# Kernel optimization log

Measured on AMD Instinct MI355X. Metric: run time of the kernel, lower is better.

## Reference

```python
import jax, jax.numpy as jnp
import numpy as np

EPS = 1.1920929e-7  # torch.finfo(float32).eps, default for F.rms_norm
ATTN_SCALE = 0.1
ROPE_BASE = 10000.0


def _rms_norm(x):
    # F.rms_norm over last dim, no learned weight
    return x * jax.lax.rsqrt(jnp.mean(x * x, axis=-1, keepdims=True) + EPS)


def _rotary(x):
    # x: [B, T, H, D]; rotates halves as in the Rotary module
    T, D = x.shape[1], x.shape[3]
    half = D // 2
    inv_freq = 1.0 / (ROPE_BASE ** (jnp.arange(0, D, 2, dtype=jnp.float32) / D))  # [half]
    freqs = jnp.arange(T, dtype=jnp.float32)[:, None] * inv_freq[None, :]          # [T, half]
    cos = jnp.cos(freqs)[None, :, None, :]
    sin = jnp.sin(freqs)[None, :, None, :]
    x1, x2 = x[..., :half], x[..., half:]
    return jnp.concatenate([x1 * cos + x2 * sin, -x1 * sin + x2 * cos], axis=-1)


def setup_inputs() -> dict:
    key = jax.random.key(0)
    ks = jax.random.split(key, 8)
    B, T, dim, H, hd = 2, 2048, 1024, 16, 64
    gate_in = 12
    s = 1.0 / np.sqrt(dim)
    return {
        "x": jax.random.normal(ks[0], (B, T, dim), dtype=jnp.float32),
        "v1": jax.random.normal(ks[1], (B, T, H, hd), dtype=jnp.float32),
        "Wq": jax.random.uniform(ks[2], (dim, dim), jnp.float32, -s, s),
        "Wk": jax.random.uniform(ks[3], (dim, dim), jnp.float32, -s, s),
        "Wv": jax.random.uniform(ks[4], (dim, dim), jnp.float32, -s, s),
        "Wproj": jax.random.uniform(ks[5], (dim, dim), jnp.float32, -s, s),
        "Wg": jax.random.uniform(ks[6], (H, gate_in), jnp.float32,
                                  -1.0 / np.sqrt(gate_in), 1.0 / np.sqrt(gate_in)),
        "lamb": jnp.float32(0.5),
    }


def reference(x, v1, Wq, Wk, Wv, Wproj, Wg, lamb):
    B, T, dim = x.shape
    H, hd = v1.shape[2], v1.shape[3]
    q = (x @ Wq.T).reshape(B, T, H, hd)
    k = (x @ Wk.T).reshape(B, T, H, hd)
    v = (x @ Wv.T).reshape(B, T, H, hd)
    # value-residual mixing
    v = (1.0 - lamb) * v + lamb * v1
    # QK RMSNorm + RoPE
    q = _rotary(_rms_norm(q))
    k = _rotary(_rms_norm(k))
    # causal SDPA with fixed scale
    scores = jnp.einsum('bqhd,bkhd->bhqk', q, k) * ATTN_SCALE
    causal = jnp.tril(jnp.ones((T, T), dtype=bool))
    scores = jnp.where(causal[None, None], scores, jnp.float32(-jnp.inf))
    probs = jax.nn.softmax(scores, axis=-1)
    y = jnp.einsum('bhqk,bkhd->bqhd', probs, v)  # [B, T, H, hd]
    # sigmoid gate from first 12 channels of x
    gate = jax.nn.sigmoid(x[..., :Wg.shape[1]] @ Wg.T)  # [B, T, H]
    y = y * gate[..., None]
    y = y.reshape(B, T, H * hd) @ Wproj.T
    return y
```

## Files before the change

kernel.cpp:

```cpp
#include <hip/hip_runtime.h>
#include <math.h>


#define B_    2
#define T_    2048
#define DIM_  1024
#define H_    16
#define HD_   64
#define NROW  (B_ * T_)
#define EPS_  1.1920929e-07f
#define SCALE_ 0.1f
#define LOG2_10K 13.287712379549449f
#define INV2PI 0.15915494309189535f

typedef unsigned short u16;
typedef unsigned int   u32;
typedef __bf16 bf16x8 __attribute__((ext_vector_type(8)));
typedef __bf16 bf16x2 __attribute__((ext_vector_type(2)));
typedef float  f32x4  __attribute__((ext_vector_type(4)));

__device__ __forceinline__ u16 f2b(float f) {
  u32 u = __float_as_uint(f);
  u += 0x7fffu + ((u >> 16) & 1u);
  return (u16)(u >> 16);
}
__device__ __forceinline__ u32 pk2(float a, float b) {
#if __has_builtin(__builtin_amdgcn_cvt_pk_bf16_f32)
  bf16x2 r = __builtin_amdgcn_cvt_pk_bf16_f32(a, b);
  return __builtin_bit_cast(u32, r);
#else
  return (u32)f2b(a) | ((u32)f2b(b) << 16);
#endif
}
__device__ __forceinline__ void fast_sincos_rev(float rev, float* s, float* c) {
  const float r = rev - floorf(rev);
#if __has_builtin(__builtin_amdgcn_sinf) && __has_builtin(__builtin_amdgcn_cosf)
  *s = __builtin_amdgcn_sinf(r);
  *c = __builtin_amdgcn_cosf(r);
#else
  *s = __sinf(r * 6.283185307179586f);
  *c = __cosf(r * 6.283185307179586f);
#endif
}
#define MFMA16(a,b,c) __builtin_amdgcn_mfma_f32_16x16x32_bf16((a),(b),(c),0,0,0)

typedef const __attribute__((address_space(1))) unsigned char gbuf_t;
typedef __attribute__((address_space(3))) unsigned char lbuf_t;
__device__ __forceinline__ void gload_lds16(const u16* g, unsigned char* l) {
  __builtin_amdgcn_global_load_lds((gbuf_t*)g, (lbuf_t*)l, 16, 0, 0);
}

__global__ __launch_bounds__(256) void convert_all(
    const float* __restrict__ x, const float* __restrict__ Wq,
    const float* __restrict__ Wk, const float* __restrict__ Wv,
    const float* __restrict__ Wp,
    u16* __restrict__ xb, u16* __restrict__ wb ) {
  const int i = blockIdx.x * 256 + threadIdx.x;
  const float* src;
  u16* dst;
  int off;
  if (i < 1048576)       { src = x;  dst = xb;            off = i; }
  else if (i < 1310720)  { src = Wq; dst = wb;            off = i - 1048576; }
  else if (i < 1572864)  { src = Wk; dst = wb + 1048576;  off = i - 1310720; }
  else if (i < 1835008)  { src = Wv; dst = wb + 2097152;  off = i - 1572864; }
  else                   { src = Wp; dst = wb + 3145728;  off = i - 1835008; }
  const float4 f = ((const float4*)src)[off];
  uint2 o;
  o.x = pk2(f.x, f.y);
  o.y = pk2(f.z, f.w);
  ((uint2*)dst)[off] = o;
}

template <bool IS_PROJ>
__global__ __launch_bounds__(256) void gemm_rp(
    const u16* __restrict__ Ab, const u16* __restrict__ Wb,
    u16* __restrict__ qo, u16* __restrict__ ko, u16* __restrict__ vto,
    float* __restrict__ fo, const float* __restrict__ v1,
    const float* __restrict__ lambp) {
  __shared__ __attribute__((aligned(16))) unsigned char sm[49152];
  const int tid  = threadIdx.x;
  const int w    = tid >> 6;
  const int lane = tid & 63;
  const int lo = lane & 15, hi = lane >> 4;
  const int raw = blockIdx.x;
  const int xcd = raw & 7;
  const int jj  = raw >> 3;
  const int m0 = (xcd * 4 + (jj & 3)) << 7;
  const int by = jj >> 2;
  const int mode = IS_PROJ ? 3 : (by >> 3);
  const int n0 = IS_PROJ ? (by << 7) : ((by & 7) << 7);
  const u16* W = IS_PROJ ? Wb : (Wb + (size_t)mode * (DIM_ * DIM_));

  const int wm = w & 1, wn = w >> 1;

  const u16* agA0 = Ab + (size_t)(m0 + (2 * w + 0) * 16 + lo) * DIM_ + (hi << 3);
  const u16* agA1 = Ab + (size_t)(m0 + (2 * w + 1) * 16 + lo) * DIM_ + (hi << 3);
  const u16* agB0 = W  + (size_t)(n0 + (2 * w + 0) * 16 + lo) * DIM_ + (hi << 3);
  const u16* agB1 = W  + (size_t)(n0 + (2 * w + 1) * 16 + lo) * DIM_ + (hi << 3);

  f32x4 acc[4][4];
#pragma unroll
  for (int i = 0; i < 4; ++i)
#pragma unroll
    for (int j = 0; j < 4; ++j) acc[i][j] = (f32x4){0.f, 0.f, 0.f, 0.f};

  {
    unsigned char* ad0 = sm + (2 * w) * 1024;
    gload_lds16(agA0, ad0);
    gload_lds16(agA1, ad0 + 1024);
    gload_lds16(agB0, ad0 + 8192);
    gload_lds16(agB1, ad0 + 9216);
    agA0 += 32; agA1 += 32; agB0 += 32; agB1 += 32;
    unsigned char* ad1 = sm + 16384 + (2 * w) * 1024;
    gload_lds16(agA0, ad1);
    gload_lds16(agA1, ad1 + 1024);
    gload_lds16(agB0, ad1 + 8192);
    gload_lds16(agB1, ad1 + 9216);
    agA0 += 32; agA1 += 32; agB0 += 32; agB1 += 32;
  }

  int cr = 0;
  int cw = 2;
  for (int kc = 0; kc < DIM_; kc += 32) {
    __builtin_amdgcn_sched_barrier(0);
    if (kc + 32 < DIM_) {
      asm volatile("s_waitcnt vmcnt(4)" ::: "memory");
    } else {
      asm volatile("s_waitcnt vmcnt(0)" ::: "memory");
    }
    __builtin_amdgcn_s_barrier();
    __builtin_amdgcn_sched_barrier(0);
    if (kc + 64 < DIM_) {
      unsigned char* ad = sm + cw * 16384 + (2 * w) * 1024;
      gload_lds16(agA0, ad);
      gload_lds16(agA1, ad + 1024);
      gload_lds16(agB0, ad + 8192);
      gload_lds16(agB1, ad + 9216);
      agA0 += 32; agA1 += 32; agB0 += 32; agB1 += 32;
    }
    const unsigned char* Acur = sm + cr * 16384;
    const unsigned char* Bcur = Acur + 8192;
    bf16x8 bfr[4];
#pragma unroll
    for (int nt = 0; nt < 4; ++nt)
      bfr[nt] = *(const bf16x8*)(Bcur + (((wn * 4 + nt) * 64 + lane) << 4));
#pragma unroll
    for (int mt = 0; mt < 4; ++mt) {
      const bf16x8 af = *(const bf16x8*)(Acur + (((wm * 4 + mt) * 64 + lane) << 4));
#pragma unroll
      for (int nt = 0; nt < 4; ++nt)
        acc[mt][nt] = MFMA16(af, bfr[nt], acc[mt][nt]);
    }
    cr = (cr == 2) ? 0 : cr + 1;
    cw = (cw == 2) ? 0 : cw + 1;
  }

  const int head = (n0 >> 6) + wn;
  if (mode <= 1) {
    u16* C = (mode == 0) ? qo : ko;
    const float if0 = exp2f(-(float)lo * (LOG2_10K / 32.f)) * INV2PI;
    const float if1 = exp2f(-(float)(lo + 16) * (LOG2_10K / 32.f)) * INV2PI;
#pragma unroll
    for (int mt = 0; mt < 4; ++mt)
#pragma unroll
      for (int r = 0; r < 4; ++r) {
        float ss = 0.f;
#pragma unroll
        for (int nt = 0; nt < 4; ++nt) { const float v = acc[mt][nt][r]; ss += v * v; }
        ss += __shfl_xor(ss, 1, 64); ss += __shfl_xor(ss, 2, 64);
        ss += __shfl_xor(ss, 4, 64); ss += __shfl_xor(ss, 8, 64);
        const float scl = rsqrtf(ss * (1.f / 64.f) + EPS_);
        const int row_g = m0 + wm * 64 + mt * 16 + hi * 4 + r;
        const float tpos = (float)(row_g & (T_ - 1));
        float sn0, cs0, sn1, cs1;
        fast_sincos_rev(tpos * if0, &sn0, &cs0);
        fast_sincos_rev(tpos * if1, &sn1, &cs1);
        u16* crow = C + (size_t)row_g * DIM_ + head * HD_;
        const float x10 = acc[mt][0][r] * scl, x11 = acc[mt][1][r] * scl;
        const float x20 = acc[mt][2][r] * scl, x21 = acc[mt][3][r] * scl;
        crow[lo]      = f2b(x10 * cs0 + x20 * sn0);
        crow[16 + lo] = f2b(x11 * cs1 + x21 * sn1);
        crow[32 + lo] = f2b(x20 * cs0 - x10 * sn0);
        crow[48 + lo] = f2b(x21 * cs1 - x11 * sn1);
      }
  } else if (mode == 2) {
    const float lam = lambp[0];
#pragma unroll
    for (int mt = 0; mt < 4; ++mt)
#pragma unroll
      for (int r = 0; r < 4; ++r) {
        const int row_g = m0 + wm * 64 + mt * 16 + hi * 4 + r;
        const int bb = row_g >> 11, tt = row_g & (T_ - 1);
        const int bh = bb * H_ + head;
        const float* v1r = v1 + (size_t)row_g * DIM_ + head * HD_;
#pragma unroll
        for (int nt = 0; nt < 4; ++nt) {
          const int d = nt * 16 + lo;
          const float ov = (1.f - lam) * acc[mt][nt][r] + lam * v1r[d];
          vto[((size_t)(bh * HD_ + d)) * T_ + tt] = f2b(ov);
        }
      }
  } else {
#pragma unroll
    for (int mt = 0; mt < 4; ++mt)
#pragma unroll
      for (int r = 0; r < 4; ++r) {
        const int row_g = m0 + wm * 64 + mt * 16 + hi * 4 + r;
        float* orow = fo + (size_t)row_g * DIM_ + n0 + wn * 64;
#pragma unroll
        for (int nt = 0; nt < 4; ++nt) orow[nt * 16 + lo] = acc[mt][nt][r];
      }
  }
}

__global__ __launch_bounds__(256) void gate_kernel(
    const float* __restrict__ x, const float* __restrict__ Wg,
    float* __restrict__ gate) {
  const int id = blockIdx.x * 256 + threadIdx.x;
  const int n = id >> 4, h = id & 15;
  const float* xr = x + (size_t)n * DIM_;
  const float* wr = Wg + h * 12;
  float s = 0.f;
#pragma unroll
  for (int j = 0; j < 12; ++j) s += xr[j] * wr[j];
  gate[id] = 1.f / (1.f + __expf(-s));
}

__global__ __launch_bounds__(256) void attn3(
    const u16* __restrict__ q, const u16* __restrict__ k, const u16* __restrict__ vt,
    const float* __restrict__ gate, u16* __restrict__ y) {
  __shared__ __attribute__((aligned(16))) unsigned char smem[49152];
  const int tid = threadIdx.x;
  const int wv = tid >> 6, lane = tid & 63, lo = lane & 15, hi = lane >> 4;
  const int raw = blockIdx.x;
  const int xcd = raw & 7;
  const int jj  = raw >> 3;
  const int qt = 31 - (jj >> 2);
  const int bh = xcd * 4 + (jj & 3);
  const int b = bh >> 4, h = bh & 15;
  const int qb = qt << 6;

  const int qrow = b * T_ + qb + wv * 16 + lo;
  const u16* qp = q + (size_t)qrow * DIM_ + h * HD_;
  const bf16x8 qf0 = *(const bf16x8*)(qp + hi * 8);
  const bf16x8 qf1 = *(const bf16x8*)(qp + 32 + hi * 8);

  f32x4 o[4];
#pragma unroll
  for (int i = 0; i < 4; ++i) o[i] = (f32x4){0.f, 0.f, 0.f, 0.f};
  float lrun = 0.f;

  const int sl = tid & 63, skh = (tid >> 6) & 1, st0 = tid >> 7;
  const int srow = sl & 15, skk = skh * 32 + ((sl >> 4) << 3);
  const u16* kg0 = k + ((size_t)(b * T_ + st0 * 16 + srow)) * DIM_ + h * HD_ + skk;
  const u16* kg1 = kg0 + (size_t)32 * DIM_;
  const u16* vg0 = vt + ((size_t)(bh * HD_ + st0 * 16 + srow)) * T_ + skk;
  const u16* vg1 = vg0 + (size_t)32 * T_;
  const int wub = (tid >> 6) << 10;

  {
    gload_lds16(kg0, smem + wub);
    gload_lds16(kg1, smem + 4096 + wub);
    gload_lds16(vg0, smem + 8192 + wub);
    gload_lds16(vg1, smem + 12288 + wub);
    const int t1 = (qt >= 1) ? 1 : 0;
    const size_t ko = (size_t)t1 * 64 * DIM_;
    const size_t vo = (size_t)t1 * 64;
    unsigned char* b1 = smem + 16384;
    gload_lds16(kg0 + ko, b1 + wub);
    gload_lds16(kg1 + ko, b1 + 4096 + wub);
    gload_lds16(vg0 + vo, b1 + 8192 + wub);
    gload_lds16(vg1 + vo, b1 + 12288 + wub);
  }

  int sr = 0, sw = 2;
  for (int tix = 0; tix <= qt; ++tix) {
    __builtin_amdgcn_sched_barrier(0);
    if (tix < qt) {
      asm volatile("s_waitcnt vmcnt(4)" ::: "memory");
    } else {
      asm volatile("s_waitcnt vmcnt(0)" ::: "memory");
    }
    __builtin_amdgcn_s_barrier();
    __builtin_amdgcn_sched_barrier(0);
    if (tix + 2 <= qt) {
      const size_t ko = (size_t)(tix + 2) * 64 * DIM_;
      const size_t vo = (size_t)(tix + 2) * 64;
      unsigned char* base = smem + sw * 16384;
      gload_lds16(kg0 + ko, base + wub);
      gload_lds16(kg1 + ko, base + 4096 + wub);
      gload_lds16(vg0 + vo, base + 8192 + wub);
      gload_lds16(vg1 + vo, base + 12288 + wub);
    }
    const unsigned char* kb = smem + sr * 16384;
    const unsigned char* vb = kb + 8192;

    f32x4 stl[4];
#pragma unroll
    for (int kt = 0; kt < 4; ++kt) stl[kt] = (f32x4){0.f, 0.f, 0.f, 0.f};
    __builtin_amdgcn_s_setprio(1);
#pragma unroll
    for (int kh = 0; kh < 2; ++kh) {
      const bf16x8 qb_ = kh ? qf1 : qf0;
#pragma unroll
      for (int kt = 0; kt < 4; ++kt) {
        const bf16x8 af = *(const bf16x8*)(kb + (((kt * 2 + kh) * 64 + lane) << 4));
        stl[kt] = MFMA16(af, qb_, stl[kt]);
      }
    }
    __builtin_amdgcn_s_setprio(0);
    const bool diag = (tix == qt);
    float ps = 0.f;
#pragma unroll
    for (int kt = 0; kt < 4; ++kt)
#pragma unroll
      for (int r = 0; r < 4; ++r) {
        float s = stl[kt][r] * SCALE_;
        if (diag && (kt * 16 + hi * 4 + r > wv * 16 + lo)) s = -3e38f;
        const float e = __expf(s);
        stl[kt][r] = e;
        ps += e;
      }
    ps += __shfl_xor(ps, 16, 64);
    ps += __shfl_xor(ps, 32, 64);
    lrun += ps;

    u32 pkv[4][2];
#pragma unroll
    for (int kt = 0; kt < 4; ++kt) {
      pkv[kt][0] = pk2(stl[kt][0], stl[kt][1]);
      pkv[kt][1] = pk2(stl[kt][2], stl[kt][3]);
    }
#pragma unroll
    for (int kh = 0; kh < 2; ++kh) {
      uint4 w4;
      u32* w4p = (u32*)&w4;
#pragma unroll
      for (int wd = 0; wd < 4; ++wd) {
        const int src = (2 * (hi & 1) + (wd >> 1)) * 16 + lo;
        const u32 a  = (u32)__shfl((int)pkv[2 * kh][wd & 1], src, 64);
        const u32 bb = (u32)__shfl((int)pkv[2 * kh + 1][wd & 1], src, 64);
        w4p[wd] = (hi < 2) ? a : bb;
      }
      const bf16x8 pf = __builtin_bit_cast(bf16x8, w4);
      __builtin_amdgcn_s_setprio(1);
#pragma unroll
      for (int dt = 0; dt < 4; ++dt) {
        const bf16x8 vf = *(const bf16x8*)(vb + (((dt * 2 + kh) * 64 + lane) << 4));
        o[dt] = MFMA16(vf, pf, o[dt]);
      }
      __builtin_amdgcn_s_setprio(0);
    }
    sr = (sr == 2) ? 0 : sr + 1;
    sw = (sw == 2) ? 0 : sw + 1;
  }

  const float inv = gate[(size_t)qrow * H_ + h] / lrun;
  u16* yrow = y + (size_t)qrow * DIM_ + h * HD_;
#pragma unroll
  for (int dt = 0; dt < 4; ++dt) {
    ushort4 pq;
    pq.x = f2b(o[dt][0] * inv); pq.y = f2b(o[dt][1] * inv);
    pq.z = f2b(o[dt][2] * inv); pq.w = f2b(o[dt][3] * inv);
    *(ushort4*)(yrow + dt * 16 + hi * 4) = pq;
  }
}

extern "C" void kernel_launch(void* const* d_in, const int* in_sizes, int n_in,
                              void* d_out, int out_size, void* d_ws, size_t ws_size,
                              hipStream_t stream) {
  const float* x    = (const float*)d_in[0];
  const float* v1   = (const float*)d_in[1];
  const float* Wq   = (const float*)d_in[2];
  const float* Wk   = (const float*)d_in[3];
  const float* Wv   = (const float*)d_in[4];
  const float* Wp   = (const float*)d_in[5];
  const float* Wg   = (const float*)d_in[6];
  const float* lamb = (const float*)d_in[7];

  const size_t NX = (size_t)NROW * DIM_;
  const size_t NW = (size_t)DIM_ * DIM_;

  u16* q  = (u16*)d_ws;
  u16* k  = q + NX;
  u16* vt = k + NX;
  u16* xb = vt + NX;
  u16* wb = xb + NX;
  float* gate = (float*)(wb + 4 * NW);

  const dim3 bb(256);

  convert_all<<<dim3(8192), bb, 0, stream>>>(x, Wq, Wk, Wv, Wp, xb, wb);
  gemm_rp<false><<<dim3(768), bb, 0, stream>>>(
      xb, wb, q, k, vt, nullptr, v1, lamb);
  gate_kernel<<<dim3(NROW * H_ / 256), bb, 0, stream>>>(x, Wg, gate);
  attn3<<<dim3(1024), bb, 0, stream>>>(q, k, vt, gate, q);
  gemm_rp<true><<<dim3(256), bb, 0, stream>>>(
      q, wb + 3 * NW, nullptr, nullptr, nullptr, (float*)d_out, nullptr, nullptr);
}
```

Measured before the change: 221.0 us.

## Pre-tile GEMM operands into MFMA fragment layout and load directly to registers

The convert kernel now writes x and the weights in a tiled layout of 16-row by 8-column fragments that matches the MFMA operand layout. The attention output is written in the same tiled layout into the xb buffer. Both GEMMs then drop LDS staging and barriers and load fragments straight from global memory into registers, double-buffered in even/odd k-steps. This removes LDS traffic and block-level syncs, but every wave now fetches its own operand tiles from global memory or cache with no sharing through LDS. Register pressure also rises.

```diff
diff --git a/kernel.cpp b/kernel.cpp
--- a/kernel.cpp
+++ b/kernel.cpp
@@ -54,21 +54,28 @@
     const float* __restrict__ x, const float* __restrict__ Wq,
     const float* __restrict__ Wk, const float* __restrict__ Wv,
     const float* __restrict__ Wp,
-    u16* __restrict__ xb, u16* __restrict__ wb ) {
+    u16* __restrict__ xb, u16* __restrict__ wb) {
   const int i = blockIdx.x * 256 + threadIdx.x;
   const float* src;
   u16* dst;
   int off;
-  if (i < 1048576)       { src = x;  dst = xb;            off = i; }
-  else if (i < 1310720)  { src = Wq; dst = wb;            off = i - 1048576; }
-  else if (i < 1572864)  { src = Wk; dst = wb + 1048576;  off = i - 1310720; }
-  else if (i < 1835008)  { src = Wv; dst = wb + 2097152;  off = i - 1572864; }
-  else                   { src = Wp; dst = wb + 3145728;  off = i - 1835008; }
-  const float4 f = ((const float4*)src)[off];
-  uint2 o;
-  o.x = pk2(f.x, f.y);
-  o.y = pk2(f.z, f.w);
-  ((uint2*)dst)[off] = o;
+  if (i < 524288) { src = x; dst = xb; off = i; }
+  else {
+    const int j = i - 524288;
+    const int s = j >> 17;
+    off = j & 131071;
+    src = (s == 0) ? Wq : (s == 1) ? Wk : (s == 2) ? Wv : Wp;
+    dst = wb + (size_t)s * 1048576;
+  }
+  const int blk = off >> 6, ln = off & 63;
+  const int row = ((blk >> 5) << 4) + (ln & 15);
+  const int col = ((blk & 31) << 5) + ((ln >> 4) << 3);
+  const float4 f0 = *(const float4*)(src + (size_t)row * DIM_ + col);
+  const float4 f1 = *(const float4*)(src + (size_t)row * DIM_ + col + 4);
+  uint4 o;
+  o.x = pk2(f0.x, f0.y); o.y = pk2(f0.z, f0.w);
+  o.z = pk2(f1.x, f1.y); o.w = pk2(f1.z, f1.w);
+  ((uint4*)dst)[off] = o;
 }
 
 template <bool IS_PROJ>
@@ -77,7 +84,6 @@
     u16* __restrict__ qo, u16* __restrict__ ko, u16* __restrict__ vto,
     float* __restrict__ fo, const float* __restrict__ v1,
     const float* __restrict__ lambp) {
-  __shared__ __attribute__((aligned(16))) unsigned char sm[49152];
   const int tid  = threadIdx.x;
   const int w    = tid >> 6;
   const int lane = tid & 63;
@@ -90,13 +96,10 @@
   const int mode = IS_PROJ ? 3 : (by >> 3);
   const int n0 = IS_PROJ ? (by << 7) : ((by & 7) << 7);
   const u16* W = IS_PROJ ? Wb : (Wb + (size_t)mode * (DIM_ * DIM_));
-
   const int wm = w & 1, wn = w >> 1;
 
-  const u16* agA0 = Ab + (size_t)(m0 + (2 * w + 0) * 16 + lo) * DIM_ + (hi << 3);
-  const u16* agA1 = Ab + (size_t)(m0 + (2 * w + 1) * 16 + lo) * DIM_ + (hi << 3);
-  const u16* agB0 = W  + (size_t)(n0 + (2 * w + 0) * 16 + lo) * DIM_ + (hi << 3);
-  const u16* agB1 = W  + (size_t)(n0 + (2 * w + 1) * 16 + lo) * DIM_ + (hi << 3);
+  const u16* pA = Ab + (size_t)((m0 >> 4) + wm * 4) * 16384 + lane * 8;
+  const u16* pB = W  + (size_t)((n0 >> 4) + wn * 4) * 16384 + lane * 8;
 
   f32x4 acc[4][4];
 #pragma unroll
@@ -104,55 +107,34 @@
 #pragma unroll
     for (int j = 0; j < 4; ++j) acc[i][j] = (f32x4){0.f, 0.f, 0.f, 0.f};
 
-  {
-    unsigned char* ad0 = sm + (2 * w) * 1024;
-    gload_lds16(agA0, ad0);
-    gload_lds16(agA1, ad0 + 1024);
-    gload_lds16(agB0, ad0 + 8192);
-    gload_lds16(agB1, ad0 + 9216);
-    agA0 += 32; agA1 += 32; agB0 += 32; agB1 += 32;
-    unsigned char* ad1 = sm + 16384 + (2 * w) * 1024;
-    gload_lds16(agA0, ad1);
-    gload_lds16(agA1, ad1 + 1024);
-    gload_lds16(agB0, ad1 + 8192);
-    gload_lds16(agB1, ad1 + 9216);
-    agA0 += 32; agA1 += 32; agB0 += 32; agB1 += 32;
-  }
-
-  int cr = 0;
-  int cw = 2;
-  for (int kc = 0; kc < DIM_; kc += 32) {
-    __builtin_amdgcn_sched_barrier(0);
-    if (kc + 32 < DIM_) {
-      asm volatile("s_waitcnt vmcnt(4)" ::: "memory");
-    } else {
-      asm volatile("s_waitcnt vmcnt(0)" ::: "memory");
-    }
-    __builtin_amdgcn_s_barrier();
-    __builtin_amdgcn_sched_barrier(0);
-    if (kc + 64 < DIM_) {
-      unsigned char* ad = sm + cw * 16384 + (2 * w) * 1024;
-      gload_lds16(agA0, ad);
-      gload_lds16(agA1, ad + 1024);
-      gload_lds16(agB0, ad + 8192);
-      gload_lds16(agB1, ad + 9216);
-      agA0 += 32; agA1 += 32; agB0 += 32; agB1 += 32;
-    }
-    const unsigned char* Acur = sm + cr * 16384;
-    const unsigned char* Bcur = Acur + 8192;
-    bf16x8 bfr[4];
-#pragma unroll
-    for (int nt = 0; nt < 4; ++nt)
-      bfr[nt] = *(const bf16x8*)(Bcur + (((wn * 4 + nt) * 64 + lane) << 4));
-#pragma unroll
-    for (int mt = 0; mt < 4; ++mt) {
-      const bf16x8 af = *(const bf16x8*)(Acur + (((wm * 4 + mt) * 64 + lane) << 4));
+  bf16x8 aE[4], bE[4], aO[4], bO[4];
+#pragma unroll
+  for (int t = 0; t < 4; ++t) {
+    aE[t] = *(const bf16x8*)(pA + t * 16384);
+    bE[t] = *(const bf16x8*)(pB + t * 16384);
+  }
+  for (int ks = 0; ks < 32; ks += 2) {
+#pragma unroll
+    for (int t = 0; t < 4; ++t) {
+      aO[t] = *(const bf16x8*)(pA + t * 16384 + (ks + 1) * 512);
+      bO[t] = *(const bf16x8*)(pB + t * 16384 + (ks + 1) * 512);
+    }
+#pragma unroll
+    for (int mt = 0; mt < 4; ++mt)
 #pragma unroll
       for (int nt = 0; nt < 4; ++nt)
-        acc[mt][nt] = MFMA16(af, bfr[nt], acc[mt][nt]);
-    }
-    cr = (cr == 2) ? 0 : cr + 1;
-    cw = (cw == 2) ? 0 : cw + 1;
+        acc[mt][nt] = MFMA16(aE[mt], bE[nt], acc[mt][nt]);
+    const int kn = (ks + 2 < 32) ? (ks + 2) : 0;
+#pragma unroll
+    for (int t = 0; t < 4; ++t) {
+      aE[t] = *(const bf16x8*)(pA + t * 16384 + kn * 512);
+      bE[t] = *(const bf16x8*)(pB + t * 16384 + kn * 512);
+    }
+#pragma unroll
+    for (int mt = 0; mt < 4; ++mt)
+#pragma unroll
+      for (int nt = 0; nt < 4; ++nt)
+        acc[mt][nt] = MFMA16(aO[mt], bO[nt], acc[mt][nt]);
   }
 
   const int head = (n0 >> 6) + wn;
@@ -228,7 +210,7 @@
 
 __global__ __launch_bounds__(256) void attn3(
     const u16* __restrict__ q, const u16* __restrict__ k, const u16* __restrict__ vt,
-    const float* __restrict__ gate, u16* __restrict__ y) {
+    const float* __restrict__ gate, u16* __restrict__ yt) {
   __shared__ __attribute__((aligned(16))) unsigned char smem[49152];
   const int tid = threadIdx.x;
   const int wv = tid >> 6, lane = tid & 63, lo = lane & 15, hi = lane >> 4;
@@ -356,13 +338,15 @@
   }
 
   const float inv = gate[(size_t)qrow * H_ + h] / lrun;
-  u16* yrow = y + (size_t)qrow * DIM_ + h * HD_;
+  u16* ybase = yt + (size_t)(qrow >> 4) * 16384 + (size_t)(h * 2) * 512
+             + lo * 8 + (hi & 1) * 4;
 #pragma unroll
   for (int dt = 0; dt < 4; ++dt) {
     ushort4 pq;
     pq.x = f2b(o[dt][0] * inv); pq.y = f2b(o[dt][1] * inv);
     pq.z = f2b(o[dt][2] * inv); pq.w = f2b(o[dt][3] * inv);
-    *(ushort4*)(yrow + dt * 16 + hi * 4) = pq;
+    const int c = (dt * 2 + (hi >> 1)) & 3;
+    *(ushort4*)(ybase + (dt >> 1) * 512 + c * 128) = pq;
   }
 }
 
@@ -390,11 +374,11 @@
 
   const dim3 bb(256);
 
-  convert_all<<<dim3(8192), bb, 0, stream>>>(x, Wq, Wk, Wv, Wp, xb, wb);
+  convert_all<<<dim3(4096), bb, 0, stream>>>(x, Wq, Wk, Wv, Wp, xb, wb);
   gemm_rp<false><<<dim3(768), bb, 0, stream>>>(
       xb, wb, q, k, vt, nullptr, v1, lamb);
   gate_kernel<<<dim3(NROW * H_ / 256), bb, 0, stream>>>(x, Wg, gate);
-  attn3<<<dim3(1024), bb, 0, stream>>>(q, k, vt, gate, q);
+  attn3<<<dim3(1024), bb, 0, stream>>>(q, k, vt, gate, xb);
   gemm_rp<true><<<dim3(256), bb, 0, stream>>>(
-      q, wb + 3 * NW, nullptr, nullptr, nullptr, (float*)d_out, nullptr, nullptr);
-}
+      xb, wb + 3 * NW, nullptr, nullptr, nullptr, (float*)d_out, nullptr, nullptr);
+}
```

New measurement: 211.2 us. 1.05x faster.

## Pre-tile Wproj and attention output into MFMA fragment layout for LDS-free projection GEMM

Applied to the files above, without the earlier changes.

The conversion kernel now writes Wproj in a 16x32 MFMA-fragment tiled layout, and the attention kernel writes its output into the same tiled layout (into xb rather than over q). This lets the new gemm_proj load operand fragments straight from global memory into registers with double buffering and no LDS staging or barriers. The attention scale is folded into q at the QKV epilogue so the softmax loop drops a multiply, and the causal mask is only evaluated on diagonal tiles. The QKV GEMM loses its XCD-aware block swizzle in favour of a plain 2D grid, which may reduce L2 locality.

```diff
diff --git a/kernel.cpp b/kernel.cpp
--- a/kernel.cpp
+++ b/kernel.cpp
@@ -54,43 +54,47 @@
     const float* __restrict__ x, const float* __restrict__ Wq,
     const float* __restrict__ Wk, const float* __restrict__ Wv,
     const float* __restrict__ Wp,
-    u16* __restrict__ xb, u16* __restrict__ wb ) {
+    u16* __restrict__ xb, u16* __restrict__ wb) {
   const int i = blockIdx.x * 256 + threadIdx.x;
-  const float* src;
-  u16* dst;
-  int off;
-  if (i < 1048576)       { src = x;  dst = xb;            off = i; }
-  else if (i < 1310720)  { src = Wq; dst = wb;            off = i - 1048576; }
-  else if (i < 1572864)  { src = Wk; dst = wb + 1048576;  off = i - 1310720; }
-  else if (i < 1835008)  { src = Wv; dst = wb + 2097152;  off = i - 1572864; }
-  else                   { src = Wp; dst = wb + 3145728;  off = i - 1835008; }
-  const float4 f = ((const float4*)src)[off];
-  uint2 o;
-  o.x = pk2(f.x, f.y);
-  o.y = pk2(f.z, f.w);
-  ((uint2*)dst)[off] = o;
-}
-
-template <bool IS_PROJ>
-__global__ __launch_bounds__(256) void gemm_rp(
+  if (i < 1835008) {
+    const float* src; u16* dst; int off;
+    if (i < 1048576)      { src = x;  dst = xb;           off = i; }
+    else if (i < 1310720) { src = Wq; dst = wb;           off = i - 1048576; }
+    else if (i < 1572864) { src = Wk; dst = wb + 1048576; off = i - 1310720; }
+    else                  { src = Wv; dst = wb + 2097152; off = i - 1572864; }
+    const float4 f = ((const float4*)src)[off];
+    uint2 o;
+    o.x = pk2(f.x, f.y);
+    o.y = pk2(f.z, f.w);
+    ((uint2*)dst)[off] = o;
+  } else {
+    const int off = i - 1835008;
+    const int blk = off >> 6, ln = off & 63;
+    const int row = ((blk >> 5) << 4) + (ln & 15);
+    const int col = ((blk & 31) << 5) + ((ln >> 4) << 3);
+    const float4 f0 = *(const float4*)(Wp + (size_t)row * DIM_ + col);
+    const float4 f1 = *(const float4*)(Wp + (size_t)row * DIM_ + col + 4);
+    uint4 o;
+    o.x = pk2(f0.x, f0.y); o.y = pk2(f0.z, f0.w);
+    o.z = pk2(f1.x, f1.y); o.w = pk2(f1.z, f1.w);
+    ((uint4*)(wb + 3145728))[off] = o;
+  }
+}
+
+__global__ __launch_bounds__(256) void gemm_qkv(
     const u16* __restrict__ Ab, const u16* __restrict__ Wb,
     u16* __restrict__ qo, u16* __restrict__ ko, u16* __restrict__ vto,
-    float* __restrict__ fo, const float* __restrict__ v1,
-    const float* __restrict__ lambp) {
+    const float* __restrict__ v1, const float* __restrict__ lambp) {
   __shared__ __attribute__((aligned(16))) unsigned char sm[49152];
   const int tid  = threadIdx.x;
   const int w    = tid >> 6;
   const int lane = tid & 63;
   const int lo = lane & 15, hi = lane >> 4;
-  const int raw = blockIdx.x;
-  const int xcd = raw & 7;
-  const int jj  = raw >> 3;
-  const int m0 = (xcd * 4 + (jj & 3)) << 7;
-  const int by = jj >> 2;
-  const int mode = IS_PROJ ? 3 : (by >> 3);
-  const int n0 = IS_PROJ ? (by << 7) : ((by & 7) << 7);
-  const u16* W = IS_PROJ ? Wb : (Wb + (size_t)mode * (DIM_ * DIM_));
-
+  const int m0 = blockIdx.x << 7;
+  const int by = blockIdx.y;
+  const int mode = by >> 3;
+  const int n0 = (by & 7) << 7;
+  const u16* W = Wb + (size_t)mode * (DIM_ * DIM_);
   const int wm = w & 1, wn = w >> 1;
 
   const u16* agA0 = Ab + (size_t)(m0 + (2 * w + 0) * 16 + lo) * DIM_ + (hi << 3);
@@ -119,8 +123,7 @@
     agA0 += 32; agA1 += 32; agB0 += 32; agB1 += 32;
   }
 
-  int cr = 0;
-  int cw = 2;
+  int cr = 0, cw = 2;
   for (int kc = 0; kc < DIM_; kc += 32) {
     __builtin_amdgcn_sched_barrier(0);
     if (kc + 32 < DIM_) {
@@ -169,7 +172,8 @@
         for (int nt = 0; nt < 4; ++nt) { const float v = acc[mt][nt][r]; ss += v * v; }
         ss += __shfl_xor(ss, 1, 64); ss += __shfl_xor(ss, 2, 64);
         ss += __shfl_xor(ss, 4, 64); ss += __shfl_xor(ss, 8, 64);
-        const float scl = rsqrtf(ss * (1.f / 64.f) + EPS_);
+        float scl = rsqrtf(ss * (1.f / 64.f) + EPS_);
+        if (mode == 0) scl *= SCALE_;
         const int row_g = m0 + wm * 64 + mt * 16 + hi * 4 + r;
         const float tpos = (float)(row_g & (T_ - 1));
         float sn0, cs0, sn1, cs1;
@@ -183,7 +187,7 @@
         crow[32 + lo] = f2b(x20 * cs0 - x10 * sn0);
         crow[48 + lo] = f2b(x21 * cs1 - x11 * sn1);
       }
-  } else if (mode == 2) {
+  } else {
     const float lam = lambp[0];
 #pragma unroll
     for (int mt = 0; mt < 4; ++mt)
@@ -200,17 +204,71 @@
           vto[((size_t)(bh * HD_ + d)) * T_ + tt] = f2b(ov);
         }
       }
-  } else {
+  }
+}
+
+__global__ __launch_bounds__(256) void gemm_proj(
+    const u16* __restrict__ Ab, const u16* __restrict__ Wb,
+    float* __restrict__ fo) {
+  const int tid  = threadIdx.x;
+  const int w    = tid >> 6;
+  const int lane = tid & 63;
+  const int lo = lane & 15, hi = lane >> 4;
+  const int raw = blockIdx.x;
+  const int xcd = raw & 7;
+  const int jj  = raw >> 3;
+  const int m0 = (xcd * 4 + (jj & 3)) << 7;
+  const int n0 = (jj >> 2) << 7;
+  const int wm = w & 1, wn = w >> 1;
+
+  const u16* pA = Ab + (size_t)((m0 >> 4) + wm * 4) * 16384 + lane * 8;
+  const u16* pB = Wb + (size_t)((n0 >> 4) + wn * 4) * 16384 + lane * 8;
+
+  f32x4 acc[4][4];
+#pragma unroll
+  for (int i = 0; i < 4; ++i)
+#pragma unroll
+    for (int j = 0; j < 4; ++j) acc[i][j] = (f32x4){0.f, 0.f, 0.f, 0.f};
+
+  bf16x8 aE[4], bE[4], aO[4], bO[4];
+#pragma unroll
+  for (int t = 0; t < 4; ++t) {
+    aE[t] = *(const bf16x8*)(pA + t * 16384);
+    bE[t] = *(const bf16x8*)(pB + t * 16384);
+  }
+  for (int ks = 0; ks < 32; ks += 2) {
+#pragma unroll
+    for (int t = 0; t < 4; ++t) {
+      aO[t] = *(const bf16x8*)(pA + t * 16384 + (ks + 1) * 512);
+      bO[t] = *(const bf16x8*)(pB + t * 16384 + (ks + 1) * 512);
+    }
 #pragma unroll
     for (int mt = 0; mt < 4; ++mt)
 #pragma unroll
-      for (int r = 0; r < 4; ++r) {
-        const int row_g = m0 + wm * 64 + mt * 16 + hi * 4 + r;
-        float* orow = fo + (size_t)row_g * DIM_ + n0 + wn * 64;
-#pragma unroll
-        for (int nt = 0; nt < 4; ++nt) orow[nt * 16 + lo] = acc[mt][nt][r];
-      }
-  }
+      for (int nt = 0; nt < 4; ++nt)
+        acc[mt][nt] = MFMA16(aE[mt], bE[nt], acc[mt][nt]);
+    const int kn = (ks + 2 < 32) ? (ks + 2) : 0;
+#pragma unroll
+    for (int t = 0; t < 4; ++t) {
+      aE[t] = *(const bf16x8*)(pA + t * 16384 + kn * 512);
+      bE[t] = *(const bf16x8*)(pB + t * 16384 + kn * 512);
+    }
+#pragma unroll
+    for (int mt = 0; mt < 4; ++mt)
+#pragma unroll
+      for (int nt = 0; nt < 4; ++nt)
+        acc[mt][nt] = MFMA16(aO[mt], bO[nt], acc[mt][nt]);
+  }
+
+#pragma unroll
+  for (int mt = 0; mt < 4; ++mt)
+#pragma unroll
+    for (int r = 0; r < 4; ++r) {
+      const int row_g = m0 + wm * 64 + mt * 16 + hi * 4 + r;
+      float* orow = fo + (size_t)row_g * DIM_ + n0 + wn * 64;
+#pragma unroll
+      for (int nt = 0; nt < 4; ++nt) orow[nt * 16 + lo] = acc[mt][nt][r];
+    }
 }
 
 __global__ __launch_bounds__(256) void gate_kernel(
@@ -228,7 +286,7 @@
 
 __global__ __launch_bounds__(256) void attn3(
     const u16* __restrict__ q, const u16* __restrict__ k, const u16* __restrict__ vt,
-    const float* __restrict__ gate, u16* __restrict__ y) {
+    const float* __restrict__ gate, u16* __restrict__ yt) {
   __shared__ __attribute__((aligned(16))) unsigned char smem[49152];
   const int tid = threadIdx.x;
   const int wv = tid >> 6, lane = tid & 63, lo = lane & 15, hi = lane >> 4;
@@ -309,18 +367,28 @@
       }
     }
     __builtin_amdgcn_s_setprio(0);
-    const bool diag = (tix == qt);
     float ps = 0.f;
-#pragma unroll
-    for (int kt = 0; kt < 4; ++kt)
-#pragma unroll
-      for (int r = 0; r < 4; ++r) {
-        float s = stl[kt][r] * SCALE_;
-        if (diag && (kt * 16 + hi * 4 + r > wv * 16 + lo)) s = -3e38f;
-        const float e = __expf(s);
-        stl[kt][r] = e;
-        ps += e;
-      }
+    if (tix != qt) {
+#pragma unroll
+      for (int kt = 0; kt < 4; ++kt)
+#pragma unroll
+        for (int r = 0; r < 4; ++r) {
+          const float e = __expf(stl[kt][r]);
+          stl[kt][r] = e;
+          ps += e;
+        }
+    } else {
+#pragma unroll
+      for (int kt = 0; kt < 4; ++kt)
+#pragma unroll
+        for (int r = 0; r < 4; ++r) {
+          float s = stl[kt][r];
+          if (kt * 16 + hi * 4 + r > wv * 16 + lo) s = -3e38f;
+          const float e = __expf(s);
+          stl[kt][r] = e;
+          ps += e;
+        }
+    }
     ps += __shfl_xor(ps, 16, 64);
     ps += __shfl_xor(ps, 32, 64);
     lrun += ps;
@@ -356,13 +424,15 @@
   }
 
   const float inv = gate[(size_t)qrow * H_ + h] / lrun;
-  u16* yrow = y + (size_t)qrow * DIM_ + h * HD_;
+  u16* ybase = yt + (size_t)(qrow >> 4) * 16384 + (size_t)(h * 2) * 512
+             + lo * 8 + (hi & 1) * 4;
 #pragma unroll
   for (int dt = 0; dt < 4; ++dt) {
     ushort4 pq;
     pq.x = f2b(o[dt][0] * inv); pq.y = f2b(o[dt][1] * inv);
     pq.z = f2b(o[dt][2] * inv); pq.w = f2b(o[dt][3] * inv);
-    *(ushort4*)(yrow + dt * 16 + hi * 4) = pq;
+    const int c = (dt * 2 + (hi >> 1)) & 3;
+    *(ushort4*)(ybase + (dt >> 1) * 512 + c * 128) = pq;
   }
 }
 
@@ -390,11 +460,9 @@
 
   const dim3 bb(256);
 
-  convert_all<<<dim3(8192), bb, 0, stream>>>(x, Wq, Wk, Wv, Wp, xb, wb);
-  gemm_rp<false><<<dim3(768), bb, 0, stream>>>(
-      xb, wb, q, k, vt, nullptr, v1, lamb);
+  convert_all<<<dim3(7680), bb, 0, stream>>>(x, Wq, Wk, Wv, Wp, xb, wb);
+  gemm_qkv<<<dim3(32, 24), bb, 0, stream>>>(xb, wb, q, k, vt, v1, lamb);
   gate_kernel<<<dim3(NROW * H_ / 256), bb, 0, stream>>>(x, Wg, gate);
-  attn3<<<dim3(1024), bb, 0, stream>>>(q, k, vt, gate, q);
-  gemm_rp<true><<<dim3(256), bb, 0, stream>>>(
-      q, wb + 3 * NW, nullptr, nullptr, nullptr, (float*)d_out, nullptr, nullptr);
-}
+  attn3<<<dim3(1024), bb, 0, stream>>>(q, k, vt, gate, xb);
+  gemm_proj<<<dim3(256), bb, 0, stream>>>(xb, wb + 3 * NW, (float*)d_out);
+}
```

New measurement: 222.1 us. Within noise of the previous version (+0.5%).
